# Optimization experiments

Hardware: AMD Instinct MI355X
Metric: run time of the kernel (lower is better)

## Reference

```python
import jax, jax.numpy as jnp
import numpy as np
import math

TOP_K = 3
LN_EPS = 1e-5


def _conv2d(x, w, b):
    # x: (1, C_in, T, p), w: (C_out, C_in, 3, 3) OIHW, padding=1 -> SAME
    y = jax.lax.conv_general_dilated(
        x, w, window_strides=(1, 1), padding=[(1, 1), (1, 1)],
        dimension_numbers=('NCHW', 'OIHW', 'NCHW'))
    return y + b[None, :, None, None]


def _dominant_periods(x, top_k):
    # fft over channel-mean series, drop DC, take top-k frequency indices + 1
    fft_vals = jnp.abs(jnp.fft.rfft(x.mean(-1), axis=-1))  # (B, L//2+1)
    fft_vals = fft_vals.at[:, 0].set(0.0)
    idx = jax.lax.top_k(fft_vals, top_k)[1] + 1  # (B, top_k)
    return np.asarray(idx)  # concrete ints: periods are data-dependent shapes


def setup_inputs() -> dict:
    key = jax.random.key(0)
    ks = jax.random.split(key, 3)
    B, L, D, C = 64, 1024, 256, 128
    return {
        'x': jax.random.normal(ks[0], (B, L, D), jnp.float32),
        'W1': jax.random.normal(ks[1], (C, D, 3, 3), jnp.float32) * 0.02,
        'b1': jnp.zeros((C,), jnp.float32),
        'W2': jax.random.normal(ks[2], (D, C, 3, 3), jnp.float32) * 0.02,
        'b2': jnp.zeros((D,), jnp.float32),
        'gamma': jnp.ones((D,), jnp.float32),
        'beta': jnp.zeros((D,), jnp.float32),
    }


def reference(x, W1, b1, W2, b2, gamma, beta):
    B, L, D = x.shape
    periods = _dominant_periods(x, TOP_K)  # (B, TOP_K) concrete
    outs = []
    for bi in range(B):
        acc = jnp.zeros((L, D), x.dtype)
        for p in periods[bi]:
            p = int(p)
            if p <= 1:
                continue
            T = math.ceil(L / p)
            pad = T * p - L
            # (D, L) -> pad -> (1, D, T, p)
            xi = jnp.pad(x[bi].T, ((0, 0), (0, pad))).reshape(1, D, T, p)
            xi = _conv2d(xi, W1, b1)
            xi = jax.nn.gelu(xi, approximate=False)  # torch GELU is exact
            xi = _conv2d(xi, W2, b2)
            xi = xi.reshape(1, D, T * p)[..., :L]
            acc = acc + xi[0].T
        outs.append(acc)
    out = jnp.stack(outs) / TOP_K
    y = x + out
    mu = y.mean(-1, keepdims=True)
    var = y.var(-1, keepdims=True)
    yn = (y - mu) * jax.lax.rsqrt(var + LN_EPS)
    return yn * gamma + beta
```

## Files before the change

### kernel.cpp

```cpp
#include <hip/hip_runtime.h>
#include <hip/hip_bf16.h>
#include <math.h>

#define B_ 64
#define L_ 1024
#define D_ 256
#define C_ 128
#define LPMAX 1536

typedef __bf16 bf16x8 __attribute__((ext_vector_type(8)));
typedef float f32x16 __attribute__((ext_vector_type(16)));

__device__ __forceinline__ unsigned short f2bf(float f) {
    __hip_bfloat16 h = __float2bfloat16(f);
    return __builtin_bit_cast(unsigned short, h);
}

__device__ __forceinline__ float gelu_exact(float f) {
    return 0.5f * f * (1.0f + erff(f * 0.70710678118654752440f));
}

__device__ __forceinline__ void gl16(const unsigned short* g, unsigned short* l) {
    __builtin_amdgcn_global_load_lds(
        (const __attribute__((address_space(1))) unsigned int*)g,
        (__attribute__((address_space(3))) unsigned int*)l, 16, 0, 0);
}

__global__ void prep_kernel(const float* __restrict__ x, unsigned short* __restrict__ xb,
                            float* __restrict__ series) {
    int row = blockIdx.x * 4 + (threadIdx.x >> 6);
    int lane = threadIdx.x & 63;
    size_t base = (size_t)row * D_ + lane * 4;
    float4 v = *reinterpret_cast<const float4*>(x + base);
    ushort4 o;
    o.x = f2bf(v.x); o.y = f2bf(v.y); o.z = f2bf(v.z); o.w = f2bf(v.w);
    *reinterpret_cast<ushort4*>(xb + base) = o;
    float s = v.x + v.y + v.z + v.w;
    #pragma unroll
    for (int d = 32; d; d >>= 1) s += __shfl_xor(s, d);
    if (lane == 0) series[row] = s * (1.0f / D_);
}

__global__ void tw_kernel(double* __restrict__ tw) {
    int j = blockIdx.x * 256 + threadIdx.x;
    if (j < 1024) {
        double a = -2.0 * 3.14159265358979323846 * (double)j / 1024.0;
        tw[2 * j] = cos(a);
        tw[2 * j + 1] = sin(a);
    }
}

__global__ void repack_kernel(const float* __restrict__ W1, const float* __restrict__ W2,
                              unsigned short* __restrict__ W1s, unsigned short* __restrict__ W2s) {
    int i = blockIdx.x * 256 + threadIdx.x;
    if (i < 294912) {
        int img = i >> 12;
        int tap = img >> 3, kk = img & 7;
        int within = i & 4095;
        int rb = within >> 9, q = (within >> 7) & 3, rr = (within >> 3) & 15, e = i & 7;
        int c = rb * 16 + rr, d = kk * 32 + q * 8 + e;
        int dt = tap / 3, dp = tap % 3;
        W1s[i] = f2bf(W1[((c * D_ + d) * 3 + dt) * 3 + dp]);
    } else {
        int i2 = i - 294912;
        if (i2 < 294912) {
            int img = i2 >> 13;
            int tap = img >> 2, kk = img & 3;
            int within = i2 & 8191;
            int rb = within >> 9, q = (within >> 7) & 3, rr = (within >> 3) & 15, e = i2 & 7;
            int dout = rb * 16 + rr, cin = kk * 32 + q * 8 + e;
            int dt = tap / 3, dp = tap % 3;
            W2s[i2] = f2bf(W2[((dout * C_ + cin) * 3 + dt) * 3 + dp]);
        }
    }
}

__global__ void dft_kernel(const float* __restrict__ series, const double* __restrict__ tw,
                           float* __restrict__ mag2) {
    int bk = blockIdx.x;
    int k = bk % 513, b = bk / 513;
    int lane = threadIdx.x;
    const float* s = series + (size_t)b * L_;
    double re = 0.0, im = 0.0;
    #pragma unroll 4
    for (int i = 0; i < 16; i++) {
        int l = lane + 64 * i;
        int idx = (k * l) & 1023;
        double sv = (double)s[l];
        re += sv * tw[2 * idx];
        im += sv * tw[2 * idx + 1];
    }
    #pragma unroll
    for (int d = 32; d; d >>= 1) { re += __shfl_down(re, d); im += __shfl_down(im, d); }
    if (lane == 0) mag2[bk] = (k == 0) ? 0.0f : (float)(re * re + im * im);
}

__global__ void topk_kernel(const float* __restrict__ mag2, int* __restrict__ periods) {
    int b = blockIdx.x;
    int lane = threadIdx.x;
    const float* m = mag2 + b * 513;
    float v[9]; int kid[9];
    #pragma unroll
    for (int r = 0; r < 9; r++) {
        int k = r * 64 + lane;
        kid[r] = k;
        v[r] = (k < 513) ? m[k] : -1.0f;
    }
    int s0 = -1, s1 = -1;
    for (int j = 0; j < 3; j++) {
        float best = -1.0f; int bi = 0x7fffffff;
        #pragma unroll
        for (int r = 0; r < 9; r++) {
            bool skip = (kid[r] == s0) || (kid[r] == s1) || (kid[r] >= 513);
            if (!skip && (v[r] > best || (v[r] == best && kid[r] < bi))) { best = v[r]; bi = kid[r]; }
        }
        #pragma unroll
        for (int d = 32; d; d >>= 1) {
            float ov = __shfl_xor(best, d);
            int oi = __shfl_xor(bi, d);
            if (ov > best || (ov == best && oi < bi)) { best = ov; bi = oi; }
        }
        if (lane == 0) periods[b * 3 + j] = bi + 1;
        if (j == 0) s0 = bi; else if (j == 1) s1 = bi;
    }
}

__global__ __launch_bounds__(256, 3)
void conv1_kernel(const unsigned short* __restrict__ xb,
                  const unsigned short* __restrict__ W1s,
                  const float* __restrict__ b1,
                  const int* __restrict__ periods,
                  unsigned short* __restrict__ out1g) {
    __shared__ __align__(16) unsigned short sA[12288];
    __shared__ __align__(16) unsigned short sB[2][5632];

    const int blk = blockIdx.x;
    const int xcd = blk & 7;
    const int li = blk >> 3;
    const int b = xcd * 8 + li / 36;
    const int rem = li % 36;
    const int j = rem / 12, tile = rem % 12;

    const int p = periods[b * 3 + j];
    if (p <= 1) return;
    const int T = (L_ + p - 1) / p;
    const int Lp = T * p;
    const int col0 = tile * 128;
    if (col0 >= Lp) return;

    const int tid = threadIdx.x;
    const int w = tid >> 6, lane = tid & 63;
    const int wm = w >> 1, wn = w & 1;
    const int l15 = lane & 15, l4 = lane >> 4;
    const int l31 = lane & 31, lh = lane >> 5;
    const int s0w = (w < 2) ? w * 3 : 6 + (w - 2) * 2;
    const int nsw = (w < 2) ? 3 : 2;

    const unsigned short* xbb = xb + (size_t)b * L_ * D_;

    int cols2[2], ppv2[2], ttv2[2];
    #pragma unroll
    for (int ci = 0; ci < 2; ci++) {
        cols2[ci] = col0 + wn * 64 + ci * 32 + l31;
        ppv2[ci] = cols2[ci] % p;
        ttv2[ci] = cols2[ci] / p;
    }

    int arow32[2];
    #pragma unroll
    for (int ri = 0; ri < 2; ri++)
        arow32[ri] = (wm * 4 + ri * 2 + (l31 >> 4)) * 512 + lh * 128 + (l31 & 15) * 8;
    const int zoff32 = 10 * 512 + lh * 128 + (l31 & 15) * 8;

    f32x16 acc00 = {0.f}, acc01 = {0.f}, acc10 = {0.f}, acc11 = {0.f};

    {
        int bf = tid >> 7, r = tid & 127;
        ushort4 z = {0, 0, 0, 0};
        *reinterpret_cast<ushort4*>(&sB[bf][10 * 512 + r * 4]) = z;
    }

    int locv[3][2];
    auto setmask = [&](int dt) {
        #pragma unroll
        for (int dp = 0; dp < 3; dp++)
            #pragma unroll
            for (int ci = 0; ci < 2; ci++) {
                int pd = ppv2[ci] + dp, td = ttv2[ci] + dt;
                int t = cols2[ci] + (dt - 1) * p + dp - 1;
                bool ok = (pd >= 1) && (pd <= p) && (td >= 1) && (td <= T) &&
                          (cols2[ci] < Lp) && (t < L_);
                int rc = wn * 64 + ci * 32 + 15 + dp + l31;
                int off = (rc >> 4) * 512 + lh * 128 + (rc & 15) * 8;
                locv[dp][ci] = ok ? off : zoff32;
            }
    };

    const unsigned short* gaB[3];
    auto setaddrB = [&](int dt) {
        const int win1 = col0 + (dt - 1) * p - 16;
        #pragma unroll
        for (int i = 0; i < 3; i++) {
            int c = win1 + (s0w + i) * 16 + l15;
            c = c < 0 ? 0 : (c > L_ - 1 ? L_ - 1 : c);
            gaB[i] = xbb + (size_t)c * D_ + l4 * 8;
        }
    };

    auto stageB = [&](int buf, int kk) {
        unsigned short* lb = sB[buf];
        #pragma unroll
        for (int i = 0; i < 3; i++)
            if (i < nsw) gl16(gaB[i] + kk * 32, lb + (s0w + i) * 512);
    };

    auto stageA = [&](int dt, int kk) {
        #pragma unroll
        for (int s6 = 0; s6 < 6; s6++) {
            int pi = w * 6 + s6;
            int dp = pi >> 3, sub = pi & 7;
            gl16(W1s + (size_t)((dt * 3 + dp) * 8 + kk) * 4096 + sub * 512 + lane * 8,
                 sA + pi * 512);
        }
    };

    setmask(0);
    setaddrB(0);
    stageB(0, 0);
    stageA(0, 0);
    asm volatile("s_waitcnt lgkmcnt(0)" ::: "memory");

    for (int ph = 0; ph < 24; ph++) {
        const int cur = ph & 1;
        const int pn = ph + 1;
        asm volatile("s_waitcnt vmcnt(0)" ::: "memory");
        __builtin_amdgcn_s_barrier();
        __builtin_amdgcn_sched_barrier(0);
        if (pn < 24) {
            if ((pn & 7) == 0) setaddrB(pn >> 3);
            stageB(cur ^ 1, pn & 7);
        }
        __builtin_amdgcn_sched_barrier(0);
        __builtin_amdgcn_s_setprio(1);
        {
            const unsigned short* lb = sB[cur];
            #pragma unroll
            for (int dp = 0; dp < 3; dp++) {
                #pragma unroll
                for (int ks = 0; ks < 2; ks++) {
                    bf16x8 Af0 = *reinterpret_cast<const bf16x8*>(sA + dp * 4096 + arow32[0] + ks * 256);
                    bf16x8 Af1 = *reinterpret_cast<const bf16x8*>(sA + dp * 4096 + arow32[1] + ks * 256);
                    bf16x8 Bf0 = *reinterpret_cast<const bf16x8*>(lb + locv[dp][0] + ks * 256);
                    bf16x8 Bf1 = *reinterpret_cast<const bf16x8*>(lb + locv[dp][1] + ks * 256);
                    acc00 = __builtin_amdgcn_mfma_f32_32x32x16_bf16(Af0, Bf0, acc00, 0, 0, 0);
                    acc01 = __builtin_amdgcn_mfma_f32_32x32x16_bf16(Af0, Bf1, acc01, 0, 0, 0);
                    acc10 = __builtin_amdgcn_mfma_f32_32x32x16_bf16(Af1, Bf0, acc10, 0, 0, 0);
                    acc11 = __builtin_amdgcn_mfma_f32_32x32x16_bf16(Af1, Bf1, acc11, 0, 0, 0);
                }
            }
        }
        __builtin_amdgcn_s_setprio(0);
        asm volatile("s_waitcnt lgkmcnt(0)" ::: "memory");
        __builtin_amdgcn_sched_barrier(0);
        __builtin_amdgcn_s_barrier();
        if (pn < 24) {
            stageA(pn >> 3, pn & 7);
            if ((pn & 7) == 0) setmask(pn >> 3);
        }
    }

    const size_t ob = (size_t)(b * 3 + j) * LPMAX * C_;
    const f32x16* accs[4] = { &acc00, &acc01, &acc10, &acc11 };
    #pragma unroll
    for (int ri = 0; ri < 2; ri++) {
        #pragma unroll
        for (int ci = 0; ci < 2; ci++) {
            const f32x16& a = *accs[ri * 2 + ci];
            const int c = cols2[ci];
            if (c < Lp) {
                #pragma unroll
                for (int t = 0; t < 4; t++) {
                    const int ch = wm * 64 + ri * 32 + t * 8 + 4 * lh;
                    const float4 bias = *reinterpret_cast<const float4*>(b1 + ch);
                    ushort4 o;
                    o.x = f2bf(gelu_exact(a[t * 4 + 0] + bias.x));
                    o.y = f2bf(gelu_exact(a[t * 4 + 1] + bias.y));
                    o.z = f2bf(gelu_exact(a[t * 4 + 2] + bias.z));
                    o.w = f2bf(gelu_exact(a[t * 4 + 3] + bias.w));
                    *reinterpret_cast<ushort4*>(out1g + ob + (size_t)c * C_ + ch) = o;
                }
            }
        }
    }
}

__global__ __launch_bounds__(256, 2)
void conv2_kernel(const unsigned short* __restrict__ out1g,
                  const unsigned short* __restrict__ W2s,
                  const float* __restrict__ b2,
                  const int* __restrict__ periods,
                  const float* __restrict__ x,
                  const float* __restrict__ gamma,
                  const float* __restrict__ beta,
                  float* __restrict__ yout) {
    __shared__ __align__(16) unsigned short sA[24576];
    __shared__ __align__(16) unsigned short sB[2][5632];

    const int blk = blockIdx.x;
    const int xcd = blk & 7;
    const int li = blk >> 3;
    const int b = xcd * 8 + (li >> 3);
    const int tile = li & 7;
    const int col0 = tile * 128;

    const int tid = threadIdx.x;
    const int w = tid >> 6, lane = tid & 63;
    const int wm = w >> 1, wn = w & 1;
    const int l15 = lane & 15, l4 = lane >> 4;
    const int l31 = lane & 31, lh = lane >> 5;
    const int s0w = (w < 2) ? w * 3 : 6 + (w - 2) * 2;
    const int nsw = (w < 2) ? 3 : 2;
    const int wcol = wn * 64;

    int p_all[3];
    #pragma unroll
    for (int jj = 0; jj < 3; jj++) p_all[jj] = periods[b * 3 + jj];
    const int nv = (p_all[0] > 1) + (p_all[1] > 1) + (p_all[2] > 1);

    int cols2[2];
    #pragma unroll
    for (int ci = 0; ci < 2; ci++) cols2[ci] = col0 + wcol + ci * 32 + l31;

    int arow32[4];
    #pragma unroll
    for (int ri = 0; ri < 4; ri++)
        arow32[ri] = (wm * 8 + ri * 2 + (l31 >> 4)) * 512 + lh * 128 + (l31 & 15) * 8;
    const int zoff32 = 10 * 512 + lh * 128 + (l31 & 15) * 8;

    f32x16 acc[4][2];
    #pragma unroll
    for (int ri = 0; ri < 4; ri++)
        #pragma unroll
        for (int ci = 0; ci < 2; ci++)
            acc[ri][ci] = f32x16{0.f};

    {
        int bf = tid >> 7, r = tid & 127;
        ushort4 z = {0, 0, 0, 0};
        *reinterpret_cast<ushort4*>(&sB[bf][10 * 512 + r * 4]) = z;
    }

    int locv[3][2];
    auto setmask = [&](int jn, int dt) {
        const int pj = p_all[jn];
        const int Tj = (L_ + pj - 1) / pj;
        const bool okj = pj > 1;
        #pragma unroll
        for (int dp = 0; dp < 3; dp++)
            #pragma unroll
            for (int ci = 0; ci < 2; ci++) {
                int pv = cols2[ci] % pj, tv = cols2[ci] / pj;
                int pd = pv + dp, td = tv + dt;
                bool ok = okj && (pd >= 1) && (pd <= pj) && (td >= 1) && (td <= Tj);
                int rc = wcol + ci * 32 + 15 + dp + l31;
                int off = (rc >> 4) * 512 + lh * 128 + (rc & 15) * 8;
                locv[dp][ci] = ok ? off : zoff32;
            }
    };

    const unsigned short* gaB[3];
    auto setaddrB = [&](int jn, int dt) {
        const int pj = p_all[jn];
        const unsigned short* bbj = out1g + (size_t)(b * 3 + jn) * LPMAX * C_;
        const int win1 = col0 + (dt - 1) * pj - 16;
        #pragma unroll
        for (int i = 0; i < 3; i++) {
            int c = win1 + (s0w + i) * 16 + l15;
            c = c < 0 ? 0 : (c > LPMAX - 1 ? LPMAX - 1 : c);
            gaB[i] = bbj + (size_t)c * C_ + l4 * 8;
        }
    };

    auto stageB = [&](int buf, int kk) {
        unsigned short* lb = sB[buf];
        #pragma unroll
        for (int i = 0; i < 3; i++)
            if (i < nsw) gl16(gaB[i] + kk * 32, lb + (s0w + i) * 512);
    };

    auto stageA = [&](int dt, int kk) {
        #pragma unroll
        for (int s12 = 0; s12 < 12; s12++) {
            int pi = w * 12 + s12;
            int dp = pi >> 4, sub = pi & 15;
            gl16(W2s + (size_t)((dt * 3 + dp) * 4 + kk) * 8192 + sub * 512 + lane * 8,
                 sA + pi * 512);
        }
    };

    setmask(0, 0);
    setaddrB(0, 0);
    stageB(0, 0);
    stageA(0, 0);

    for (int ph = 0; ph < 36; ph++) {
        const int cur = ph & 1;
        const int pn = ph + 1;
        asm volatile("s_waitcnt vmcnt(0)" ::: "memory");
        __builtin_amdgcn_s_barrier();
        __builtin_amdgcn_sched_barrier(0);
        if (pn < 36) {
            if ((pn & 3) == 0) setaddrB(pn / 12, (pn / 4) % 3);
            stageB(cur ^ 1, pn & 3);
        }
        __builtin_amdgcn_sched_barrier(0);
        __builtin_amdgcn_s_setprio(1);
        {
            const unsigned short* lb = sB[cur];
            #pragma unroll
            for (int dp = 0; dp < 3; dp++) {
                #pragma unroll
                for (int ks = 0; ks < 2; ks++) {
                    bf16x8 Bf0 = *reinterpret_cast<const bf16x8*>(lb + locv[dp][0] + ks * 256);
                    bf16x8 Bf1 = *reinterpret_cast<const bf16x8*>(lb + locv[dp][1] + ks * 256);
                    #pragma unroll
                    for (int ri = 0; ri < 4; ri++) {
                        bf16x8 Af = *reinterpret_cast<const bf16x8*>(sA + dp * 8192 + arow32[ri] + ks * 256);
                        acc[ri][0] = __builtin_amdgcn_mfma_f32_32x32x16_bf16(Af, Bf0, acc[ri][0], 0, 0, 0);
                        acc[ri][1] = __builtin_amdgcn_mfma_f32_32x32x16_bf16(Af, Bf1, acc[ri][1], 0, 0, 0);
                    }
                }
            }
        }
        __builtin_amdgcn_s_setprio(0);
        asm volatile("s_waitcnt lgkmcnt(0)" ::: "memory");
        __builtin_amdgcn_sched_barrier(0);
        __builtin_amdgcn_s_barrier();
        if (pn < 36) {
            stageA((pn / 4) % 3, pn & 3);
            if ((pn & 3) == 0) setmask(pn / 12, (pn / 4) % 3);
        }
    }

    const float inv3 = 1.0f / 3.0f;
    const float fnv = (float)nv;
    float sum2[2] = {0.f, 0.f}, ssq2[2] = {0.f, 0.f};
    #pragma unroll
    for (int ri = 0; ri < 4; ri++) {
        #pragma unroll
        for (int ci = 0; ci < 2; ci++) {
            const int c = cols2[ci];
            #pragma unroll
            for (int t = 0; t < 4; t++) {
                const int dout = wm * 128 + ri * 32 + t * 8 + 4 * lh;
                const float4 bb = *reinterpret_cast<const float4*>(b2 + dout);
                const size_t xoff = ((size_t)b * L_ + c) * D_ + dout;
                const float4 xr = *reinterpret_cast<const float4*>(x + xoff);
                float y0 = xr.x + (acc[ri][ci][t * 4 + 0] + fnv * bb.x) * inv3;
                float y1 = xr.y + (acc[ri][ci][t * 4 + 1] + fnv * bb.y) * inv3;
                float y2 = xr.z + (acc[ri][ci][t * 4 + 2] + fnv * bb.z) * inv3;
                float y3 = xr.w + (acc[ri][ci][t * 4 + 3] + fnv * bb.w) * inv3;
                acc[ri][ci][t * 4 + 0] = y0;
                acc[ri][ci][t * 4 + 1] = y1;
                acc[ri][ci][t * 4 + 2] = y2;
                acc[ri][ci][t * 4 + 3] = y3;
                sum2[ci] += y0 + y1 + y2 + y3;
                ssq2[ci] += y0 * y0 + y1 * y1 + y2 * y2 + y3 * y3;
            }
        }
    }
    #pragma unroll
    for (int ci = 0; ci < 2; ci++) {
        sum2[ci] += __shfl_xor(sum2[ci], 32);
        ssq2[ci] += __shfl_xor(ssq2[ci], 32);
    }
    float* red = (float*)&sB[0][0];
    if (lh == 0) {
        #pragma unroll
        for (int ci = 0; ci < 2; ci++) {
            red[((w * 2 + ci) * 32 + l31) * 2 + 0] = sum2[ci];
            red[((w * 2 + ci) * 32 + l31) * 2 + 1] = ssq2[ci];
        }
    }
    __syncthreads();
    float muv[2], invv[2];
    #pragma unroll
    for (int ci = 0; ci < 2; ci++) {
        float ts = red[((wn * 2 + ci) * 32 + l31) * 2 + 0] +
                   red[(((2 + wn) * 2 + ci) * 32 + l31) * 2 + 0];
        float tq = red[((wn * 2 + ci) * 32 + l31) * 2 + 1] +
                   red[(((2 + wn) * 2 + ci) * 32 + l31) * 2 + 1];
        float mu = ts * (1.0f / 256.0f);
        float var = tq * (1.0f / 256.0f) - mu * mu;
        muv[ci] = mu;
        invv[ci] = 1.0f / sqrtf(var + 1e-5f);
    }
    #pragma unroll
    for (int ri = 0; ri < 4; ri++) {
        #pragma unroll
        for (int ci = 0; ci < 2; ci++) {
            const int c = cols2[ci];
            const float mu = muv[ci], inv = invv[ci];
            #pragma unroll
            for (int t = 0; t < 4; t++) {
                const int dout = wm * 128 + ri * 32 + t * 8 + 4 * lh;
                const float4 g4 = *reinterpret_cast<const float4*>(gamma + dout);
                const float4 be4 = *reinterpret_cast<const float4*>(beta + dout);
                const size_t xoff = ((size_t)b * L_ + c) * D_ + dout;
                float4 o;
                o.x = (acc[ri][ci][t * 4 + 0] - mu) * inv * g4.x + be4.x;
                o.y = (acc[ri][ci][t * 4 + 1] - mu) * inv * g4.y + be4.y;
                o.z = (acc[ri][ci][t * 4 + 2] - mu) * inv * g4.z + be4.z;
                o.w = (acc[ri][ci][t * 4 + 3] - mu) * inv * g4.w + be4.w;
                *reinterpret_cast<float4*>(yout + xoff) = o;
            }
        }
    }
}

extern "C" void kernel_launch(void* const* d_in, const int* in_sizes, int n_in,
                              void* d_out, int out_size, void* d_ws, size_t ws_size,
                              hipStream_t stream) {
    const float* x     = (const float*)d_in[0];
    const float* W1    = (const float*)d_in[1];
    const float* b1    = (const float*)d_in[2];
    const float* W2    = (const float*)d_in[3];
    const float* b2    = (const float*)d_in[4];
    const float* gamma = (const float*)d_in[5];
    const float* beta  = (const float*)d_in[6];
    float* out = (float*)d_out;

    char* ws = (char*)d_ws;
    size_t off = 0;
    auto walloc = [&](size_t bytes) -> void* {
        void* pp = ws + off;
        off += (bytes + 255) & ~(size_t)255;
        return pp;
    };
    unsigned short* xb    = (unsigned short*)walloc((size_t)B_ * L_ * D_ * 2);
    unsigned short* out1g = (unsigned short*)walloc((size_t)B_ * 3 * LPMAX * C_ * 2);
    float* series         = (float*)walloc((size_t)B_ * L_ * 4);
    float* mag2           = (float*)walloc((size_t)B_ * 513 * 4);
    int* periods          = (int*)walloc((size_t)B_ * 3 * 4);
    double* tw            = (double*)walloc(1024 * 16);
    unsigned short* W1s   = (unsigned short*)walloc((size_t)294912 * 2);
    unsigned short* W2s   = (unsigned short*)walloc((size_t)294912 * 2);

    prep_kernel<<<B_ * L_ / 4, 256, 0, stream>>>(x, xb, series);
    tw_kernel<<<4, 256, 0, stream>>>(tw);
    repack_kernel<<<2304, 256, 0, stream>>>(W1, W2, W1s, W2s);
    dft_kernel<<<B_ * 513, 64, 0, stream>>>(series, tw, mag2);
    topk_kernel<<<B_, 64, 0, stream>>>(mag2, periods);
    conv1_kernel<<<B_ * 3 * 12, 256, 0, stream>>>(xb, W1s, b1, periods, out1g);
    conv2_kernel<<<B_ * 8, 256, 0, stream>>>(out1g, W2s, b2, periods, x, gamma, beta, out);
}
```

Before: 361.9 us.

## Pipeline conv1 weight staging per dp-slice with triple-buffered LDS ring

Restructures the conv1 main loop from 24 phases (each loading all three dp weight slices, then computing) into 72 finer steps. Each step computes one dp slice while weight tiles for two steps ahead are prefetched into a three-slot LDS ring, and staging of the B (input) tile is issued once per group. A second barrier and the lgkmcnt wait per phase are removed and replaced by counted vmcnt waits, aiming to overlap global→LDS loads with MFMA work. Every wave now issues three B loads instead of the former 3/3/2/2 split, so ranges overlap (wave 3 starts at slot 7 and reaches 9). The result depends on the precise vmcnt counts, and a miscount could cause data races.

```diff
diff --git a/kernel.cpp b/kernel.cpp
--- a/kernel.cpp
+++ b/kernel.cpp
@@ -131,7 +131,7 @@
                   const float* __restrict__ b1,
                   const int* __restrict__ periods,
                   unsigned short* __restrict__ out1g) {
-    __shared__ __align__(16) unsigned short sA[12288];
+    __shared__ __align__(16) unsigned short sA[3][4096];
     __shared__ __align__(16) unsigned short sB[2][5632];
 
     const int blk = blockIdx.x;
@@ -153,8 +153,7 @@
     const int wm = w >> 1, wn = w & 1;
     const int l15 = lane & 15, l4 = lane >> 4;
     const int l31 = lane & 31, lh = lane >> 5;
-    const int s0w = (w < 2) ? w * 3 : 6 + (w - 2) * 2;
-    const int nsw = (w < 2) ? 3 : 2;
+    const int s0w = (w == 3) ? 7 : w * 3;
 
     const unsigned short* xbb = xb + (size_t)b * L_ * D_;
 
@@ -211,61 +210,67 @@
         unsigned short* lb = sB[buf];
         #pragma unroll
         for (int i = 0; i < 3; i++)
-            if (i < nsw) gl16(gaB[i] + kk * 32, lb + (s0w + i) * 512);
-    };
-
-    auto stageA = [&](int dt, int kk) {
-        #pragma unroll
-        for (int s6 = 0; s6 < 6; s6++) {
-            int pi = w * 6 + s6;
-            int dp = pi >> 3, sub = pi & 7;
-            gl16(W1s + (size_t)((dt * 3 + dp) * 8 + kk) * 4096 + sub * 512 + lane * 8,
-                 sA + pi * 512);
-        }
+            gl16(gaB[i] + kk * 32, lb + (s0w + i) * 512);
+    };
+
+    auto stageA = [&](int slot, int dt, int kk, int dp) {
+        const unsigned short* src = W1s + (size_t)((dt * 3 + dp) * 8 + kk) * 4096;
+        gl16(src + (w * 2 + 0) * 512 + lane * 8, sA[slot] + (w * 2 + 0) * 512);
+        gl16(src + (w * 2 + 1) * 512 + lane * 8, sA[slot] + (w * 2 + 1) * 512);
     };
 
     setmask(0);
     setaddrB(0);
     stageB(0, 0);
-    stageA(0, 0);
+    stageA(0, 0, 0, 0);
+    stageA(1, 0, 0, 1);
     asm volatile("s_waitcnt lgkmcnt(0)" ::: "memory");
 
-    for (int ph = 0; ph < 24; ph++) {
-        const int cur = ph & 1;
-        const int pn = ph + 1;
-        asm volatile("s_waitcnt vmcnt(0)" ::: "memory");
+    int g = 0;
+    #pragma unroll 1
+    for (int u = 0; u < 72; u++) {
+        const int pos = u - g * 3;
+        if (u == 71) {
+            asm volatile("s_waitcnt vmcnt(0)" ::: "memory");
+        } else if (u == 70) {
+            asm volatile("s_waitcnt vmcnt(2)" ::: "memory");
+        } else if (pos == 1) {
+            asm volatile("s_waitcnt vmcnt(5)" ::: "memory");
+        } else {
+            asm volatile("s_waitcnt vmcnt(2)" ::: "memory");
+        }
         __builtin_amdgcn_s_barrier();
-        __builtin_amdgcn_sched_barrier(0);
-        if (pn < 24) {
-            if ((pn & 7) == 0) setaddrB(pn >> 3);
-            stageB(cur ^ 1, pn & 7);
-        }
         __builtin_amdgcn_sched_barrier(0);
         __builtin_amdgcn_s_setprio(1);
         {
-            const unsigned short* lb = sB[cur];
+            const unsigned short* la = sA[pos];
+            const unsigned short* lb = sB[g & 1];
             #pragma unroll
-            for (int dp = 0; dp < 3; dp++) {
-                #pragma unroll
-                for (int ks = 0; ks < 2; ks++) {
-                    bf16x8 Af0 = *reinterpret_cast<const bf16x8*>(sA + dp * 4096 + arow32[0] + ks * 256);
-                    bf16x8 Af1 = *reinterpret_cast<const bf16x8*>(sA + dp * 4096 + arow32[1] + ks * 256);
-                    bf16x8 Bf0 = *reinterpret_cast<const bf16x8*>(lb + locv[dp][0] + ks * 256);
-                    bf16x8 Bf1 = *reinterpret_cast<const bf16x8*>(lb + locv[dp][1] + ks * 256);
-                    acc00 = __builtin_amdgcn_mfma_f32_32x32x16_bf16(Af0, Bf0, acc00, 0, 0, 0);
-                    acc01 = __builtin_amdgcn_mfma_f32_32x32x16_bf16(Af0, Bf1, acc01, 0, 0, 0);
-                    acc10 = __builtin_amdgcn_mfma_f32_32x32x16_bf16(Af1, Bf0, acc10, 0, 0, 0);
-                    acc11 = __builtin_amdgcn_mfma_f32_32x32x16_bf16(Af1, Bf1, acc11, 0, 0, 0);
-                }
+            for (int ks = 0; ks < 2; ks++) {
+                bf16x8 Af0 = *reinterpret_cast<const bf16x8*>(la + arow32[0] + ks * 256);
+                bf16x8 Af1 = *reinterpret_cast<const bf16x8*>(la + arow32[1] + ks * 256);
+                bf16x8 Bf0 = *reinterpret_cast<const bf16x8*>(lb + locv[pos][0] + ks * 256);
+                bf16x8 Bf1 = *reinterpret_cast<const bf16x8*>(lb + locv[pos][1] + ks * 256);
+                acc00 = __builtin_amdgcn_mfma_f32_32x32x16_bf16(Af0, Bf0, acc00, 0, 0, 0);
+                acc01 = __builtin_amdgcn_mfma_f32_32x32x16_bf16(Af0, Bf1, acc01, 0, 0, 0);
+                acc10 = __builtin_amdgcn_mfma_f32_32x32x16_bf16(Af1, Bf0, acc10, 0, 0, 0);
+                acc11 = __builtin_amdgcn_mfma_f32_32x32x16_bf16(Af1, Bf1, acc11, 0, 0, 0);
             }
         }
         __builtin_amdgcn_s_setprio(0);
-        asm volatile("s_waitcnt lgkmcnt(0)" ::: "memory");
         __builtin_amdgcn_sched_barrier(0);
-        __builtin_amdgcn_s_barrier();
-        if (pn < 24) {
-            stageA(pn >> 3, pn & 7);
-            if ((pn & 7) == 0) setmask(pn >> 3);
+        if (pos == 0 && g + 1 < 24) {
+            const int ng = g + 1, nkk = ng & 7;
+            if (nkk == 0) setaddrB(ng >> 3);
+            stageB(ng & 1, nkk);
+        }
+        if (u + 2 < 72) {
+            const int u2 = u + 2, g2 = u2 / 3, p2 = u2 - g2 * 3;
+            stageA(p2, g2 >> 3, g2 & 7, p2);
+        }
+        if (pos == 2) {
+            if (((g + 1) & 7) == 0 && g + 1 < 24) setmask((g + 1) >> 3);
+            g++;
         }
     }
 
```

After: 398.3 us. +10.1%, slower.
